# Optimization experiments

Measured on AMD Instinct MI355X. Metric: run time of the kernel, lower is better.

Reference implementation:

```python
import jax, jax.numpy as jnp
import numpy as np

B, S, DIN, DOUT, E, K = 4, 2048, 1024, 1024, 16, 2


def setup_inputs() -> dict:
    key = jax.random.key(0)
    ks = jax.random.split(key, 6)
    sc = 1.0 / np.sqrt(DIN)
    return {
        "x": jax.random.normal(ks[0], (B, S, DIN), jnp.float32),
        "gate_w": jax.random.uniform(ks[1], (DIN, E), jnp.float32, -sc, sc),
        "gate_b": jax.random.uniform(ks[2], (E,), jnp.float32, -sc, sc),
        "expert_w": jax.random.uniform(ks[3], (E, DIN, DOUT), jnp.float32, -sc, sc),
        "expert_b": jax.random.uniform(ks[4], (E, DOUT), jnp.float32, -sc, sc),
        "expert_biases": jnp.zeros((E,), jnp.float32),
    }


def reference(x, gate_w, gate_b, expert_w, expert_b, expert_biases):
    # gating
    gate_output = x @ gate_w + gate_b                 # [B,S,E]
    gate_probs = jax.nn.sigmoid(gate_output)          # [B,S,E]
    gate_logits = gate_output + expert_biases         # bias-corrected routing logits
    _, top_k_idx = jax.lax.top_k(gate_logits, K)      # [B,S,K] int32
    top_k_probs = jnp.take_along_axis(gate_probs, top_k_idx, axis=-1)  # [B,S,K]
    top_k_probs = top_k_probs / top_k_probs.sum(-1, keepdims=True)

    # dense all-expert compute, as in the original torch.stack
    expert_outputs = jnp.einsum('bsd,edf->ebsf', x, expert_w) + expert_b[:, None, None, :]  # [E,B,S,DOUT]

    # Faithful replication of the torch gather (which, due to the permute,
    # reads channel j (0..K-1) of the selected expert and broadcasts it over DOUT):
    # out[d,b,s,j] = expert_outputs[topk[b,s,j], b, s, j]
    b_ix = jnp.arange(B)[:, None, None]
    s_ix = jnp.arange(S)[None, :, None]
    j_ix = jnp.arange(K)[None, None, :]
    gathered = expert_outputs[top_k_idx, b_ix, s_ix, j_ix]  # [B,S,K]

    final_scalar = (gathered * top_k_probs).sum(-1)          # [B,S]
    final_output = jnp.broadcast_to(final_scalar[..., None], (B, S, DOUT))
    return final_output, gate_probs, top_k_idx
```

## Files before the change

### kernel.cpp

```cpp
#include <hip/hip_runtime.h>
#include <math.h>

#define DIN_  1024
#define DOUT_ 1024
#define NE    16
#define KK    2
#define NTOK  8192


__global__ __launch_bounds__(256) void compact_w_kernel(
    const float* __restrict__ ew,
    float* __restrict__ wc)
{
    int i = blockIdx.x * 256 + threadIdx.x;
    if (i >= NE * KK * DIN_) return;
    int d = i & (DIN_ - 1);
    int j = (i >> 10) & 1;
    int e = i >> 11;
    wc[i] = ew[(size_t)e * DIN_ * DOUT_ + (size_t)d * DOUT_ + j];
}

__global__ __launch_bounds__(256) void gate_kernel(
    const float* __restrict__ x,
    const float* __restrict__ gate_w,
    const float* __restrict__ gate_b,
    const float* __restrict__ ebias,
    float* __restrict__ out_probs,
    float* __restrict__ out_idx,
    float4* __restrict__ ws_rec,
    int write_aux)
{
    __shared__ float red[NE][16][17];
    __shared__ float lgt[16 * NE];

    const int tid = threadIdx.x;
    const int seg = tid >> 4;
    const int tok = tid & 15;
    const int token = blockIdx.x * 16 + tok;

    const float4* x4  = (const float4*)(x + (size_t)token * DIN_) + seg * 16;
    const float4* gw4 = (const float4*)gate_w;

    float acc[NE];
#pragma unroll
    for (int e = 0; e < NE; e++) acc[e] = 0.f;

    for (int i = 0; i < 16; i++) {
        float4 xv = x4[i];
        int d0 = seg * 64 + i * 4;
#pragma unroll
        for (int j = 0; j < 4; j++) {
            int d = d0 + j;
            float xs = (j == 0) ? xv.x : (j == 1) ? xv.y : (j == 2) ? xv.z : xv.w;
            float4 g0 = gw4[d * 4 + 0];
            float4 g1 = gw4[d * 4 + 1];
            float4 g2 = gw4[d * 4 + 2];
            float4 g3 = gw4[d * 4 + 3];
            acc[0]  += xs * g0.x; acc[1]  += xs * g0.y; acc[2]  += xs * g0.z; acc[3]  += xs * g0.w;
            acc[4]  += xs * g1.x; acc[5]  += xs * g1.y; acc[6]  += xs * g1.z; acc[7]  += xs * g1.w;
            acc[8]  += xs * g2.x; acc[9]  += xs * g2.y; acc[10] += xs * g2.z; acc[11] += xs * g2.w;
            acc[12] += xs * g3.x; acc[13] += xs * g3.y; acc[14] += xs * g3.z; acc[15] += xs * g3.w;
        }
    }

#pragma unroll
    for (int e = 0; e < NE; e++) red[e][seg][tok] = acc[e];
    __syncthreads();

    {
        const int rtok = tid >> 4;
        const int e    = tid & 15;
        float s = 0.f;
#pragma unroll
        for (int sg = 0; sg < 16; sg++) s += red[e][sg][rtok];
        s += gate_b[e];
        float prob = 1.f / (1.f + expf(-s));
        int gtoken = blockIdx.x * 16 + rtok;
        if (write_aux) out_probs[(size_t)gtoken * NE + e] = prob;
        lgt[rtok * NE + e] = s;
    }
    __syncthreads();

    if (tid < 16) {
        const int ftok = tid;
        const int gtoken = blockIdx.x * 16 + ftok;
        float go[NE], logit[NE];
#pragma unroll
        for (int e = 0; e < NE; e++) {
            go[e] = lgt[ftok * NE + e];
            logit[e] = go[e] + ebias[e];
        }
        int i0 = 0;
        for (int e = 1; e < NE; e++) if (logit[e] > logit[i0]) i0 = e;
        int i1 = -1;
        for (int e = 0; e < NE; e++) {
            if (e == i0) continue;
            if (i1 < 0 || logit[e] > logit[i1]) i1 = e;
        }
        float p0 = 1.f / (1.f + expf(-go[i0]));
        float p1 = 1.f / (1.f + expf(-go[i1]));
        float inv = 1.f / (p0 + p1);
        if (write_aux) {
            out_idx[(size_t)gtoken * KK + 0] = (float)i0;
            out_idx[(size_t)gtoken * KK + 1] = (float)i1;
        }
        ws_rec[gtoken] = make_float4((float)i0, (float)i1, p0 * inv, p1 * inv);
    }
}

__global__ __launch_bounds__(256) void expert_kernel(
    const float* __restrict__ x,
    const float* __restrict__ wc,
    const float* __restrict__ expert_b,
    const float4* __restrict__ ws_rec,
    float* __restrict__ out_final)
{
    const int wave = threadIdx.x >> 6;
    const int lane = threadIdx.x & 63;
    const int token = blockIdx.x * 4 + wave;

    float4 rec = ws_rec[token];
    int e0 = (int)rec.x;
    int e1 = (int)rec.y;

    const float4* xr = (const float4*)(x + (size_t)token * DIN_);
    const float4* w0 = (const float4*)(wc + ((size_t)e0 * KK + 0) * DIN_);
    const float4* w1 = (const float4*)(wc + ((size_t)e1 * KK + 1) * DIN_);

    float g0 = 0.f, g1 = 0.f;
#pragma unroll
    for (int i = 0; i < 4; i++) {
        float4 xv = xr[i * 64 + lane];
        float4 a  = w0[i * 64 + lane];
        float4 b  = w1[i * 64 + lane];
        g0 += xv.x * a.x + xv.y * a.y + xv.z * a.z + xv.w * a.w;
        g1 += xv.x * b.x + xv.y * b.y + xv.z * b.z + xv.w * b.w;
    }
#pragma unroll
    for (int m = 32; m >= 1; m >>= 1) {
        g0 += __shfl_xor(g0, m, 64);
        g1 += __shfl_xor(g1, m, 64);
    }
    float f = rec.z * (g0 + expert_b[(size_t)e0 * DOUT_ + 0])
            + rec.w * (g1 + expert_b[(size_t)e1 * DOUT_ + 1]);
    float4 fv = make_float4(f, f, f, f);
    float4* o4 = (float4*)(out_final + (size_t)token * DOUT_);
#pragma unroll
    for (int i = 0; i < 4; i++) o4[i * 64 + lane] = fv;
}

extern "C" void kernel_launch(void* const* d_in, const int* in_sizes, int n_in,
                              void* d_out, int out_size, void* d_ws, size_t ws_size,
                              hipStream_t stream) {
    const float* x        = (const float*)d_in[0];
    const float* gate_w   = (const float*)d_in[1];
    const float* gate_b   = (const float*)d_in[2];
    const float* expert_w = (const float*)d_in[3];
    const float* expert_b = (const float*)d_in[4];
    const float* ebias    = (const float*)d_in[5];
    float* out = (float*)d_out;

    float4* ws_rec = (float4*)d_ws;
    float*  wc     = (float*)d_ws + (size_t)NTOK * 4;

    float* out_final = out;
    float* out_probs = out + (size_t)NTOK * DOUT_;
    float* out_idx   = out_probs + (size_t)NTOK * NE;
    int write_aux = (out_size >= NTOK * DOUT_ + NTOK * NE + NTOK * KK) ? 1 : 0;

    compact_w_kernel<<<(NE * KK * DIN_ + 255) / 256, 256, 0, stream>>>(expert_w, wc);
    gate_kernel<<<NTOK / 16, 256, 0, stream>>>(
        x, gate_w, gate_b, ebias, out_probs, out_idx, ws_rec, write_aux);
    expert_kernel<<<NTOK / 4, 256, 0, stream>>>(
        x, wc, expert_b, ws_rec, out_final);
}
```

Baseline: 157.1 us.

## Fuse gating and expert dot-product kernels, keeping x rows in registers

Merges the gate kernel and the expert kernel into one launch. Each thread loads its slice of x once into registers and reuses it for both the gate matvec and the two selected-expert dot products, so x is read from global memory once instead of twice. The routing record now passes through shared memory instead of the workspace, and the broadcast output is written per block. This adds register pressure from holding 16 float4 per thread, which may lower occupancy, and adds extra block-wide syncs.

```diff
diff --git a/kernel.cpp b/kernel.cpp
--- a/kernel.cpp
+++ b/kernel.cpp
@@ -6,6 +6,7 @@
 #define NE    16
 #define KK    2
 #define NTOK  8192
+#define TPB   16
 
 
 __global__ __launch_bounds__(256) void compact_w_kernel(
@@ -20,33 +21,41 @@
     wc[i] = ew[(size_t)e * DIN_ * DOUT_ + (size_t)d * DOUT_ + j];
 }
 
-__global__ __launch_bounds__(256) void gate_kernel(
+__global__ __launch_bounds__(256) void moe_fused_kernel(
     const float* __restrict__ x,
     const float* __restrict__ gate_w,
     const float* __restrict__ gate_b,
     const float* __restrict__ ebias,
+    const float* __restrict__ wc,
+    const float* __restrict__ expert_b,
+    float* __restrict__ out_final,
     float* __restrict__ out_probs,
     float* __restrict__ out_idx,
-    float4* __restrict__ ws_rec,
     int write_aux)
 {
     __shared__ float red[NE][16][17];
-    __shared__ float lgt[16 * NE];
+    __shared__ float lgt[TPB * NE];
+    __shared__ float4 s_rec[TPB];
+    __shared__ float s_final[TPB];
 
     const int tid = threadIdx.x;
     const int seg = tid >> 4;
     const int tok = tid & 15;
-    const int token = blockIdx.x * 16 + tok;
+    const int token = blockIdx.x * TPB + tok;
 
-    const float4* x4  = (const float4*)(x + (size_t)token * DIN_) + seg * 16;
+    const float4* x4 = (const float4*)(x + (size_t)token * DIN_) + seg * 16;
+    float4 xr[16];
+#pragma unroll
+    for (int i = 0; i < 16; i++) xr[i] = x4[i];
+
     const float4* gw4 = (const float4*)gate_w;
-
     float acc[NE];
 #pragma unroll
     for (int e = 0; e < NE; e++) acc[e] = 0.f;
 
+#pragma unroll 4
     for (int i = 0; i < 16; i++) {
-        float4 xv = x4[i];
+        float4 xv = xr[i];
         int d0 = seg * 64 + i * 4;
 #pragma unroll
         for (int j = 0; j < 4; j++) {
@@ -62,7 +71,6 @@
             acc[12] += xs * g3.x; acc[13] += xs * g3.y; acc[14] += xs * g3.z; acc[15] += xs * g3.w;
         }
     }
-
 #pragma unroll
     for (int e = 0; e < NE; e++) red[e][seg][tok] = acc[e];
     __syncthreads();
@@ -74,16 +82,17 @@
 #pragma unroll
         for (int sg = 0; sg < 16; sg++) s += red[e][sg][rtok];
         s += gate_b[e];
-        float prob = 1.f / (1.f + expf(-s));
-        int gtoken = blockIdx.x * 16 + rtok;
-        if (write_aux) out_probs[(size_t)gtoken * NE + e] = prob;
+        if (write_aux) {
+            float prob = 1.f / (1.f + expf(-s));
+            out_probs[(size_t)(blockIdx.x * TPB + rtok) * NE + e] = prob;
+        }
         lgt[rtok * NE + e] = s;
     }
     __syncthreads();
 
-    if (tid < 16) {
+    if (tid < TPB) {
         const int ftok = tid;
-        const int gtoken = blockIdx.x * 16 + ftok;
+        const int gtoken = blockIdx.x * TPB + ftok;
         float go[NE], logit[NE];
 #pragma unroll
         for (int e = 0; e < NE; e++) {
@@ -104,49 +113,50 @@
             out_idx[(size_t)gtoken * KK + 0] = (float)i0;
             out_idx[(size_t)gtoken * KK + 1] = (float)i1;
         }
-        ws_rec[gtoken] = make_float4((float)i0, (float)i1, p0 * inv, p1 * inv);
+        s_rec[ftok] = make_float4((float)i0, (float)i1, p0 * inv, p1 * inv);
     }
-}
+    __syncthreads();
 
-__global__ __launch_bounds__(256) void expert_kernel(
-    const float* __restrict__ x,
-    const float* __restrict__ wc,
-    const float* __restrict__ expert_b,
-    const float4* __restrict__ ws_rec,
-    float* __restrict__ out_final)
-{
-    const int wave = threadIdx.x >> 6;
-    const int lane = threadIdx.x & 63;
-    const int token = blockIdx.x * 4 + wave;
+    {
+        float4 rec = s_rec[tok];
+        int e0 = (int)rec.x;
+        int e1 = (int)rec.y;
+        const float4* w0 = (const float4*)(wc + ((size_t)e0 * KK + 0) * DIN_) + seg * 16;
+        const float4* w1 = (const float4*)(wc + ((size_t)e1 * KK + 1) * DIN_) + seg * 16;
+        float g0 = 0.f, g1 = 0.f;
+#pragma unroll 4
+        for (int i = 0; i < 16; i++) {
+            float4 xv = xr[i];
+            float4 a = w0[i];
+            float4 b = w1[i];
+            g0 += xv.x * a.x + xv.y * a.y + xv.z * a.z + xv.w * a.w;
+            g1 += xv.x * b.x + xv.y * b.y + xv.z * b.z + xv.w * b.w;
+        }
+        red[0][seg][tok] = g0;
+        red[1][seg][tok] = g1;
+    }
+    __syncthreads();
 
-    float4 rec = ws_rec[token];
-    int e0 = (int)rec.x;
-    int e1 = (int)rec.y;
+    if (tid < TPB) {
+        const int ftok = tid;
+        float4 rec = s_rec[ftok];
+        int e0 = (int)rec.x;
+        int e1 = (int)rec.y;
+        float g0 = 0.f, g1 = 0.f;
+#pragma unroll
+        for (int sg = 0; sg < 16; sg++) { g0 += red[0][sg][ftok]; g1 += red[1][sg][ftok]; }
+        g0 += expert_b[(size_t)e0 * DOUT_ + 0];
+        g1 += expert_b[(size_t)e1 * DOUT_ + 1];
+        s_final[ftok] = rec.z * g0 + rec.w * g1;
+    }
+    __syncthreads();
 
-    const float4* xr = (const float4*)(x + (size_t)token * DIN_);
-    const float4* w0 = (const float4*)(wc + ((size_t)e0 * KK + 0) * DIN_);
-    const float4* w1 = (const float4*)(wc + ((size_t)e1 * KK + 1) * DIN_);
-
-    float g0 = 0.f, g1 = 0.f;
-#pragma unroll
-    for (int i = 0; i < 4; i++) {
-        float4 xv = xr[i * 64 + lane];
-        float4 a  = w0[i * 64 + lane];
-        float4 b  = w1[i * 64 + lane];
-        g0 += xv.x * a.x + xv.y * a.y + xv.z * a.z + xv.w * a.w;
-        g1 += xv.x * b.x + xv.y * b.y + xv.z * b.z + xv.w * b.w;
+    float4* ob = (float4*)(out_final + (size_t)blockIdx.x * TPB * DOUT_);
+#pragma unroll 4
+    for (int k = 0; k < TPB; k++) {
+        float f = s_final[k];
+        ob[k * (DOUT_ / 4) + tid] = make_float4(f, f, f, f);
     }
-#pragma unroll
-    for (int m = 32; m >= 1; m >>= 1) {
-        g0 += __shfl_xor(g0, m, 64);
-        g1 += __shfl_xor(g1, m, 64);
-    }
-    float f = rec.z * (g0 + expert_b[(size_t)e0 * DOUT_ + 0])
-            + rec.w * (g1 + expert_b[(size_t)e1 * DOUT_ + 1]);
-    float4 fv = make_float4(f, f, f, f);
-    float4* o4 = (float4*)(out_final + (size_t)token * DOUT_);
-#pragma unroll
-    for (int i = 0; i < 4; i++) o4[i * 64 + lane] = fv;
 }
 
 extern "C" void kernel_launch(void* const* d_in, const int* in_sizes, int n_in,
@@ -160,8 +170,7 @@
     const float* ebias    = (const float*)d_in[5];
     float* out = (float*)d_out;
 
-    float4* ws_rec = (float4*)d_ws;
-    float*  wc     = (float*)d_ws + (size_t)NTOK * 4;
+    float* wc = (float*)d_ws;
 
     float* out_final = out;
     float* out_probs = out + (size_t)NTOK * DOUT_;
@@ -169,8 +178,7 @@
     int write_aux = (out_size >= NTOK * DOUT_ + NTOK * NE + NTOK * KK) ? 1 : 0;
 
     compact_w_kernel<<<(NE * KK * DIN_ + 255) / 256, 256, 0, stream>>>(expert_w, wc);
-    gate_kernel<<<NTOK / 16, 256, 0, stream>>>(
-        x, gate_w, gate_b, ebias, out_probs, out_idx, ws_rec, write_aux);
-    expert_kernel<<<NTOK / 4, 256, 0, stream>>>(
-        x, wc, expert_b, ws_rec, out_final);
+    moe_fused_kernel<<<NTOK / TPB, 256, 0, stream>>>(
+        x, gate_w, gate_b, ebias, wc, expert_b,
+        out_final, out_probs, out_idx, write_aux);
 }
```

Result: slower. 180.7 us (+15.1%).
